# Optimization experiments

Measured on AMD Instinct MI355X. Metric: run time of the kernel, lower is better.

The kernel has to match this reference:

```python
import jax, jax.numpy as jnp
import numpy as np

# Model config (matches init_kwargs)
DIM = 2048
INTER = 1408          # moe_inter_dim
E = 16                # n_routed_experts
TOPK = 4              # n_activated_experts
G = 4                 # n_expert_groups
TOPK_G = 2            # n_limited_groups
N_SHARED = 2
SHARED_INTER = N_SHARED * INTER  # 2816
ROUTE_SCALE = 1.0


def setup_inputs() -> dict:
    key = jax.random.key(0)
    ks = jax.random.split(key, 8)
    s = 0.02
    x = jax.random.normal(ks[0], (1, 2048, DIM), dtype=jnp.float32)
    Wg = jax.random.normal(ks[1], (E, DIM), dtype=jnp.float32) * s      # gate weight
    W1 = jax.random.normal(ks[2], (E, INTER, DIM), dtype=jnp.float32) * s  # expert gate proj
    W3 = jax.random.normal(ks[3], (E, INTER, DIM), dtype=jnp.float32) * s  # expert up proj
    W2 = jax.random.normal(ks[4], (E, DIM, INTER), dtype=jnp.float32) * s  # expert down proj
    Ws1 = jax.random.normal(ks[5], (SHARED_INTER, DIM), dtype=jnp.float32) * s
    Ws3 = jax.random.normal(ks[6], (SHARED_INTER, DIM), dtype=jnp.float32) * s
    Ws2 = jax.random.normal(ks[7], (DIM, SHARED_INTER), dtype=jnp.float32) * s
    return {"x": x, "Wg": Wg, "W1": W1, "W3": W3, "W2": W2,
            "Ws1": Ws1, "Ws3": Ws3, "Ws2": Ws2}


def _moe_forward(x, Wg, W1, W3, W2, Ws1, Ws3, Ws2):
    B, S, D = x.shape
    xt = x.reshape(-1, D)              # [T, D]
    T = xt.shape[0]

    # ---- Gate: group-limited top-k routing (bias is None since dim != 7168) ----
    scores = jax.nn.softmax(xt @ Wg.T, axis=-1)          # [T, E]
    sg = scores.reshape(T, G, E // G)                    # [T, G, E/G]
    group_scores = sg.max(axis=-1)                       # amax per group
    gidx = jax.lax.top_k(group_scores, TOPK_G)[1]        # [T, TOPK_G]
    gmask = jax.nn.one_hot(gidx, G, dtype=jnp.float32).sum(axis=1) > 0  # [T, G] kept groups
    masked = jnp.where(gmask[:, :, None], sg, -jnp.inf).reshape(T, E)
    topi = jax.lax.top_k(masked, TOPK)[1]                # [T, TOPK] expert indices
    weights = jnp.take_along_axis(scores, topi, axis=1) * ROUTE_SCALE  # original_scores gather

    # ---- Routed experts: dense per-expert SwiGLU FFN, zero-weight combine ----
    # combine[t, e] = sum over k of weights[t, k] * (topi[t, k] == e)
    combine = jnp.zeros((T, E), xt.dtype).at[jnp.arange(T)[:, None], topi].add(weights)
    h = jax.nn.silu(jnp.einsum('td,eid->eti', xt, W1)) * jnp.einsum('td,eid->eti', xt, W3)
    expert_out = jnp.einsum('eti,edi->etd', h, W2)       # [E, T, D]
    y = jnp.einsum('etd,te->td', expert_out, combine)    # [T, D]

    # ---- Shared expert (applied to all tokens) ----
    z = (jax.nn.silu(xt @ Ws1.T) * (xt @ Ws3.T)) @ Ws2.T

    return (y + z).reshape(B, S, D)


def reference(x, Wg, W1, W3, W2, Ws1, Ws3, Ws2):
    return _moe_forward(x, Wg, W1, W3, W2, Ws1, Ws3, Ws2)
```

## Files before the change

### kernel.cpp

```cpp
#include <hip/hip_runtime.h>
#include <stdint.h>

#define D_MODEL  2048
#define N_INTER  1408
#define SH_INTER 2816
#define T_TOK    2048
#define NSLOT    (T_TOK * 4)
#define MIB(x)   ((size_t)(x) << 20)

typedef __attribute__((ext_vector_type(8))) short bf16x8;
typedef __attribute__((ext_vector_type(4))) float f32x4;

__device__ __forceinline__ unsigned short f2bf(float f){
  unsigned int b = __builtin_bit_cast(unsigned int, f);
  b = (b + 0x7FFFu + ((b >> 16) & 1u)) >> 16;
  return (unsigned short)b;
}
__device__ __forceinline__ float bf2f(unsigned short h){
  unsigned int b = ((unsigned int)h) << 16;
  return __builtin_bit_cast(float, b);
}

#define GLOAD16(gp, lp) __builtin_amdgcn_global_load_lds( \
    (const __attribute__((address_space(1))) unsigned int*)(gp), \
    (__attribute__((address_space(3))) unsigned int*)(lp), 16, 0, 0)

__global__ void cvt_bf16_kernel(const float* __restrict__ x,
                                unsigned short* __restrict__ o, int n4){
  const int stride = gridDim.x * blockDim.x;
  for (int i = blockIdx.x * blockDim.x + threadIdx.x; i < n4; i += stride){
    const float4 v = ((const float4*)x)[i];
    ushort4 u; u.x = f2bf(v.x); u.y = f2bf(v.y); u.z = f2bf(v.z); u.w = f2bf(v.w);
    ((ushort4*)o)[i] = u;
  }
}

__global__ void gate_kernel(const float* __restrict__ x, const float* __restrict__ Wg,
                            int* __restrict__ cnt, int* __restrict__ list,
                            float* __restrict__ wslot){
  const int t = blockIdx.x;
  const int l = threadIdx.x;
  const int e = l & 15, q = l >> 4;
  const float* xr = x + (size_t)t * D_MODEL + q * 512;
  const float* wr = Wg + (size_t)e * D_MODEL + q * 512;
  float p = 0.f;
  #pragma unroll 4
  for (int i = 0; i < 512; i += 4){
    float4 xv = *(const float4*)(xr + i);
    float4 wv = *(const float4*)(wr + i);
    p += xv.x*wv.x + xv.y*wv.y + xv.z*wv.z + xv.w*wv.w;
  }
  p += __shfl_xor(p, 16);
  p += __shfl_xor(p, 32);
  float mx = p;
  for (int d = 1; d < 16; d <<= 1) mx = fmaxf(mx, __shfl_xor(mx, d));
  float ex = __expf(p - mx);
  float sum = ex;
  for (int d = 1; d < 16; d <<= 1) sum += __shfl_xor(sum, d);
  const float sc = ex / sum;
  float gm = fmaxf(sc, __shfl_xor(sc, 1));
  gm = fmaxf(gm, __shfl_xor(gm, 2));
  const float g0 = __shfl(gm, 0), g1 = __shfl(gm, 4),
              g2 = __shfl(gm, 8), g3 = __shfl(gm, 12);
  const int grp = e >> 2;
  const float gs[4] = {g0, g1, g2, g3};
  int grank = 0;
  #pragma unroll
  for (int j = 0; j < 4; ++j)
    if (gs[j] > gm || (gs[j] == gm && j < grp)) grank++;
  const float msc = (grank < 2) ? sc : -INFINITY;
  int erank = 0;
  #pragma unroll
  for (int j = 0; j < 16; ++j){
    const float oj = __shfl(msc, j);
    if (oj > msc || (oj == msc && j < e)) erank++;
  }
  if (q == 0 && erank < 4 && msc > -INFINITY){
    const int pos = atomicAdd(&cnt[e], 1);
    const int slot = (t << 2) | erank;
    list[e * T_TOK + pos] = slot;
    wslot[slot] = sc;
  }
}

template<int GATHER>
__global__ __launch_bounds__(256, 2)
void gemm_gu_kernel(const unsigned short* __restrict__ A,
                    const unsigned short* __restrict__ BG,
                    const unsigned short* __restrict__ BU,
                    unsigned short* __restrict__ H,
                    const int* __restrict__ list,
                    const int* __restrict__ cnt,
                    int ebase, int K, int NI, int MT, int NT)
{
  __shared__ __align__(128) char smem[24576 + 49152];
  unsigned short* As = (unsigned short*)smem;
  unsigned short* Bs = (unsigned short*)(smem + 24576);
  float* scr = (float*)smem;

  const int per = gridDim.x >> 3;
  const int gsw = (blockIdx.x & 7) * per + (blockIdx.x >> 3);
  const int mt   = gsw % MT;
  const int rest = gsw / MT;
  const int nt = GATHER ? (rest % NT) : rest;
  const int e  = GATHER ? (ebase + rest / NT) : 0;
  const int cntE = GATHER ? cnt[e] : (MT * 128);
  if (mt * 128 >= cntE) return;

  const int tid = threadIdx.x, wid = tid >> 6, lane = tid & 63;
  const int sx = ((lane & 3) ^ ((lane >> 3) & 3)) << 3;

  const int rt0 = 32 * wid + (lane >> 2), rt1 = rt0 + 16;
  int ar0, ar1;
  if (GATHER){
    const int lim = cntE - 1;
    int p0 = mt * 128 + rt0; p0 = p0 < lim ? p0 : lim;
    int p1 = mt * 128 + rt1; p1 = p1 < lim ? p1 : lim;
    ar0 = list[e * T_TOK + p0] >> 2;
    ar1 = list[e * T_TOK + p1] >> 2;
  } else { ar0 = mt * 128 + rt0; ar1 = mt * 128 + rt1; }
  const unsigned short* pa0 = A + (size_t)ar0 * K + sx;
  const unsigned short* pa1 = A + (size_t)ar1 * K + sx;

  const unsigned short* wsrc = (wid < 2) ? BG : BU;
  if (GATHER) wsrc += (size_t)(e - ebase) * NI * K;
  const int rb = (64 * wid + (lane >> 2)) & 127;
  const unsigned short* pb0 = wsrc + (size_t)(nt * 128 + rb     ) * K + sx;
  const unsigned short* pb1 = wsrc + (size_t)(nt * 128 + rb + 16) * K + sx;
  const unsigned short* pb2 = wsrc + (size_t)(nt * 128 + rb + 32) * K + sx;
  const unsigned short* pb3 = wsrc + (size_t)(nt * 128 + rb + 48) * K + sx;

  const int aW0 = (32 * wid) * 32, aW1 = aW0 + 512;
  const int bW  = (64 * wid) * 32;
  const int aStr = 128 * 32, bStr = 256 * 32;

  const int wr = wid >> 1, wc = wid & 1, lr = lane & 15, lq = lane >> 4;
  const int fx = ((lq ^ ((lr >> 1) & 3)) << 3);
  int aoff[4], boff[8];
  #pragma unroll
  for (int m = 0; m < 4; ++m) aoff[m] = (wr * 64 + m * 16 + lr) * 32 + fx;
  #pragma unroll
  for (int n = 0; n < 8; ++n) boff[n] = (wc * 128 + n * 16 + lr) * 32 + fx;

  f32x4 acc[4][8];
  const f32x4 zero = {0.f, 0.f, 0.f, 0.f};
  #pragma unroll
  for (int m = 0; m < 4; ++m)
    #pragma unroll
    for (int n = 0; n < 8; ++n) acc[m][n] = zero;

  const int KT = K >> 5;
  #pragma unroll
  for (int t = 0; t < 3; ++t){
    GLOAD16(pa0, As + t * aStr + aW0);
    GLOAD16(pa1, As + t * aStr + aW1);
    GLOAD16(pb0, Bs + t * bStr + bW);
    GLOAD16(pb1, Bs + t * bStr + bW + 512);
    GLOAD16(pb2, Bs + t * bStr + bW + 1024);
    GLOAD16(pb3, Bs + t * bStr + bW + 1536);
    pa0 += 32; pa1 += 32; pb0 += 32; pb1 += 32; pb2 += 32; pb3 += 32;
  }
  int c = 0;

  for (int kt = 0; kt < KT; ++kt){
    if (kt < KT - 2)       asm volatile("s_waitcnt vmcnt(12)" ::: "memory");
    else if (kt == KT - 2) asm volatile("s_waitcnt vmcnt(6)"  ::: "memory");
    else                   asm volatile("s_waitcnt vmcnt(0)"  ::: "memory");
    __builtin_amdgcn_s_barrier();

    const unsigned short* aC = As + c * aStr;
    const unsigned short* bC = Bs + c * bStr;
    bf16x8 af[4], bf[8];
    #pragma unroll
    for (int m = 0; m < 4; ++m) af[m] = *(const bf16x8*)(aC + aoff[m]);
    #pragma unroll
    for (int n = 0; n < 8; ++n) bf[n] = *(const bf16x8*)(bC + boff[n]);

    asm volatile("s_waitcnt lgkmcnt(0)" ::: "memory");
    __builtin_amdgcn_sched_barrier(0);
    __builtin_amdgcn_s_barrier();

    if (kt + 3 < KT){
      GLOAD16(pa0, As + c * aStr + aW0);
      GLOAD16(pa1, As + c * aStr + aW1);
      GLOAD16(pb0, Bs + c * bStr + bW);
      GLOAD16(pb1, Bs + c * bStr + bW + 512);
      GLOAD16(pb2, Bs + c * bStr + bW + 1024);
      GLOAD16(pb3, Bs + c * bStr + bW + 1536);
      pa0 += 32; pa1 += 32; pb0 += 32; pb1 += 32; pb2 += 32; pb3 += 32;
    }

    #pragma unroll
    for (int n = 0; n < 8; ++n)
      #pragma unroll
      for (int m = 0; m < 4; ++m)
        acc[m][n] = __builtin_amdgcn_mfma_f32_16x16x32_bf16(af[m], bf[n], acc[m][n], 0, 0, 0);

    c = (c == 2) ? 0 : c + 1;
  }

  if (wc == 1){
    #pragma unroll
    for (int m = 0; m < 4; ++m)
      #pragma unroll
      for (int r = 0; r < 4; ++r){
        const int row = m * 16 + lq * 4 + r;
        #pragma unroll
        for (int n = 0; n < 8; ++n){
          const int ucol = (n * 16 + lr) ^ ((lq & 1) << 4);
          scr[wr * 8192 + row * 128 + ucol] = acc[m][n][r];
        }
      }
  }
  __syncthreads();
  if (wc == 0){
    #pragma unroll
    for (int m = 0; m < 4; ++m)
      #pragma unroll
      for (int r = 0; r < 4; ++r){
        const int row = m * 16 + lq * 4 + r;
        const int grow = mt * 128 + wr * 64 + row;
        if (GATHER && grow >= cntE) continue;
        const int orow = GATHER ? list[e * T_TOK + grow] : grow;
        unsigned short* op = H + (size_t)orow * NI + nt * 128;
        #pragma unroll
        for (int n = 0; n < 8; ++n){
          const float g = acc[m][n][r];
          const int ucol = (n * 16 + lr) ^ ((lq & 1) << 4);
          const float u = scr[wr * 8192 + row * 128 + ucol];
          op[n * 16 + lr] = f2bf(g / (1.f + __expf(-g)) * u);
        }
      }
  }
}

template<int GATHER>
__global__ __launch_bounds__(256, 2)
void gemm_down_kernel(const unsigned short* __restrict__ A,
                      const unsigned short* __restrict__ B,
                      void* __restrict__ OutP,
                      const int* __restrict__ list,
                      const int* __restrict__ cnt,
                      int K, int N, int MT, int NT)
{
  __shared__ __align__(128) char smem[24576 + 49152];
  unsigned short* As = (unsigned short*)smem;
  unsigned short* Bs = (unsigned short*)(smem + 24576);

  const int per = gridDim.x >> 3;
  const int gsw = (blockIdx.x & 7) * per + (blockIdx.x >> 3);
  const int mt   = gsw % MT;
  const int rest = gsw / MT;
  const int nt = GATHER ? (rest % NT) : rest;
  const int e  = GATHER ? (rest / NT) : 0;
  const int cntE = GATHER ? cnt[e] : (MT * 128);
  if (mt * 128 >= cntE) return;

  const int tid = threadIdx.x, wid = tid >> 6, lane = tid & 63;
  const int sx = ((lane & 3) ^ ((lane >> 3) & 3)) << 3;

  const int rt0 = 32 * wid + (lane >> 2), rt1 = rt0 + 16;
  int ar0, ar1;
  if (GATHER){
    const int lim = cntE - 1;
    int p0 = mt * 128 + rt0; p0 = p0 < lim ? p0 : lim;
    int p1 = mt * 128 + rt1; p1 = p1 < lim ? p1 : lim;
    ar0 = list[e * T_TOK + p0];
    ar1 = list[e * T_TOK + p1];
  } else { ar0 = mt * 128 + rt0; ar1 = mt * 128 + rt1; }
  const unsigned short* pa0 = A + (size_t)ar0 * K + sx;
  const unsigned short* pa1 = A + (size_t)ar1 * K + sx;

  const unsigned short* wsrc = B + (GATHER ? (size_t)e * N * K : 0);
  const int rb = 64 * wid + (lane >> 2);
  const unsigned short* pb0 = wsrc + (size_t)(nt * 256 + rb     ) * K + sx;
  const unsigned short* pb1 = wsrc + (size_t)(nt * 256 + rb + 16) * K + sx;
  const unsigned short* pb2 = wsrc + (size_t)(nt * 256 + rb + 32) * K + sx;
  const unsigned short* pb3 = wsrc + (size_t)(nt * 256 + rb + 48) * K + sx;

  const int aW0 = (32 * wid) * 32, aW1 = aW0 + 512;
  const int bW  = (64 * wid) * 32;
  const int aStr = 128 * 32, bStr = 256 * 32;

  const int wr = wid >> 1, wc = wid & 1, lr = lane & 15, lq = lane >> 4;
  const int fx = ((lq ^ ((lr >> 1) & 3)) << 3);
  int aoff[4], boff[8];
  #pragma unroll
  for (int m = 0; m < 4; ++m) aoff[m] = (wr * 64 + m * 16 + lr) * 32 + fx;
  #pragma unroll
  for (int n = 0; n < 8; ++n) boff[n] = (wc * 128 + n * 16 + lr) * 32 + fx;

  f32x4 acc[4][8];
  const f32x4 zero = {0.f, 0.f, 0.f, 0.f};
  #pragma unroll
  for (int m = 0; m < 4; ++m)
    #pragma unroll
    for (int n = 0; n < 8; ++n) acc[m][n] = zero;

  const int KT = K >> 5;
  #pragma unroll
  for (int t = 0; t < 3; ++t){
    GLOAD16(pa0, As + t * aStr + aW0);
    GLOAD16(pa1, As + t * aStr + aW1);
    GLOAD16(pb0, Bs + t * bStr + bW);
    GLOAD16(pb1, Bs + t * bStr + bW + 512);
    GLOAD16(pb2, Bs + t * bStr + bW + 1024);
    GLOAD16(pb3, Bs + t * bStr + bW + 1536);
    pa0 += 32; pa1 += 32; pb0 += 32; pb1 += 32; pb2 += 32; pb3 += 32;
  }
  int c = 0;

  for (int kt = 0; kt < KT; ++kt){
    if (kt < KT - 2)       asm volatile("s_waitcnt vmcnt(12)" ::: "memory");
    else if (kt == KT - 2) asm volatile("s_waitcnt vmcnt(6)"  ::: "memory");
    else                   asm volatile("s_waitcnt vmcnt(0)"  ::: "memory");
    __builtin_amdgcn_s_barrier();

    const unsigned short* aC = As + c * aStr;
    const unsigned short* bC = Bs + c * bStr;
    bf16x8 af[4], bf[8];
    #pragma unroll
    for (int m = 0; m < 4; ++m) af[m] = *(const bf16x8*)(aC + aoff[m]);
    #pragma unroll
    for (int n = 0; n < 8; ++n) bf[n] = *(const bf16x8*)(bC + boff[n]);

    asm volatile("s_waitcnt lgkmcnt(0)" ::: "memory");
    __builtin_amdgcn_sched_barrier(0);
    __builtin_amdgcn_s_barrier();

    if (kt + 3 < KT){
      GLOAD16(pa0, As + c * aStr + aW0);
      GLOAD16(pa1, As + c * aStr + aW1);
      GLOAD16(pb0, Bs + c * bStr + bW);
      GLOAD16(pb1, Bs + c * bStr + bW + 512);
      GLOAD16(pb2, Bs + c * bStr + bW + 1024);
      GLOAD16(pb3, Bs + c * bStr + bW + 1536);
      pa0 += 32; pa1 += 32; pb0 += 32; pb1 += 32; pb2 += 32; pb3 += 32;
    }

    #pragma unroll
    for (int n = 0; n < 8; ++n)
      #pragma unroll
      for (int m = 0; m < 4; ++m)
        acc[m][n] = __builtin_amdgcn_mfma_f32_16x16x32_bf16(af[m], bf[n], acc[m][n], 0, 0, 0);

    c = (c == 2) ? 0 : c + 1;
  }

  const int colBase = nt * 256 + wc * 128;
  #pragma unroll
  for (int m = 0; m < 4; ++m){
    #pragma unroll
    for (int r = 0; r < 4; ++r){
      const int grow = mt * 128 + wr * 64 + m * 16 + lq * 4 + r;
      if (GATHER == 0){
        float* op = (float*)OutP + (size_t)grow * N + colBase;
        #pragma unroll
        for (int n = 0; n < 8; ++n) op[n * 16 + lr] = acc[m][n][r];
      } else {
        if (grow >= cntE) continue;
        const int orow = list[e * T_TOK + grow];
        unsigned short* op = (unsigned short*)OutP + (size_t)orow * N + colBase;
        #pragma unroll
        for (int n = 0; n < 8; ++n) op[n * 16 + lr] = f2bf(acc[m][n][r]);
      }
    }
  }
}

__global__ void combine_kernel(const unsigned short* __restrict__ H2,
                               const float* __restrict__ wslot,
                               float* __restrict__ out){
  const int t = blockIdx.x;
  const int ccol = threadIdx.x * 8;
  float w[4];
  #pragma unroll
  for (int k = 0; k < 4; ++k) w[k] = wslot[t * 4 + k];
  float* o = out + (size_t)t * D_MODEL + ccol;
  float a[8];
  #pragma unroll
  for (int j = 0; j < 8; ++j) a[j] = o[j];
  #pragma unroll
  for (int k = 0; k < 4; ++k){
    const bf16x8 hv = *(const bf16x8*)(H2 + (size_t)(t * 4 + k) * D_MODEL + ccol);
    #pragma unroll
    for (int j = 0; j < 8; ++j) a[j] += w[k] * bf2f((unsigned short)hv[j]);
  }
  #pragma unroll
  for (int j = 0; j < 8; ++j) o[j] = a[j];
}

extern "C" void kernel_launch(void* const* d_in, const int* in_sizes, int n_in,
                              void* d_out, int out_size, void* d_ws, size_t ws_size,
                              hipStream_t stream)
{
  const float* x   = (const float*)d_in[0];
  const float* Wg  = (const float*)d_in[1];
  const float* W1  = (const float*)d_in[2];
  const float* W3  = (const float*)d_in[3];
  const float* W2  = (const float*)d_in[4];
  const float* Ws1 = (const float*)d_in[5];
  const float* Ws3 = (const float*)d_in[6];
  const float* Ws2 = (const float*)d_in[7];
  float* out = (float*)d_out;

  char* ws = (char*)d_ws;
  int*   cnt   = (int*)(ws);
  int*   list  = (int*)(ws + 4096);
  float* wslot = (float*)(ws + 4096 + 131072);
  unsigned short* xbf = (unsigned short*)(ws + MIB(1));
  unsigned short* H2  = (unsigned short*)(ws + MIB(1));
  unsigned short* Hs  = (unsigned short*)(ws + MIB(10));
  unsigned short* Hr  = (unsigned short*)(ws + MIB(34));
  unsigned short* WA  = (unsigned short*)(ws + MIB(57));
  unsigned short* WB  = (unsigned short*)(ws + MIB(101));

  hipMemsetAsync(cnt, 0, 4096, stream);
  cvt_bf16_kernel<<<2048, 256, 0, stream>>>(x, xbf, T_TOK * D_MODEL / 4);
  gate_kernel<<<T_TOK, 64, 0, stream>>>(x, Wg, cnt, list, wslot);

  cvt_bf16_kernel<<<2048, 256, 0, stream>>>(Ws1, WA, SH_INTER * D_MODEL / 4);
  cvt_bf16_kernel<<<2048, 256, 0, stream>>>(Ws3, WB, SH_INTER * D_MODEL / 4);
  gemm_gu_kernel<0><<<16 * 22, 256, 0, stream>>>(xbf, WA, WB, Hs, nullptr, nullptr,
                                                 0, D_MODEL, SH_INTER, 16, 22);
  cvt_bf16_kernel<<<2048, 256, 0, stream>>>(Ws2, WA, D_MODEL * SH_INTER / 4);
  gemm_down_kernel<0><<<16 * 8, 256, 0, stream>>>(Hs, WA, out, nullptr, nullptr,
                                                  SH_INTER, D_MODEL, 16, 8);

  for (int h = 0; h < 2; ++h){
    const size_t wOff = (size_t)(8 * h) * N_INTER * D_MODEL;
    cvt_bf16_kernel<<<4096, 256, 0, stream>>>(W1 + wOff, WA, (int)(8u * N_INTER * D_MODEL / 4));
    cvt_bf16_kernel<<<4096, 256, 0, stream>>>(W3 + wOff, WB, (int)(8u * N_INTER * D_MODEL / 4));
    gemm_gu_kernel<1><<<16 * 11 * 8, 256, 0, stream>>>(xbf, WA, WB, Hr, list, cnt,
                                                       8 * h, D_MODEL, N_INTER, 16, 11);
  }
  cvt_bf16_kernel<<<8192, 256, 0, stream>>>(W2, WA, 16 * D_MODEL * N_INTER / 4);
  gemm_down_kernel<1><<<16 * 8 * 16, 256, 0, stream>>>(Hr, WA, H2, list, cnt,
                                                       N_INTER, D_MODEL, 16, 8);
  combine_kernel<<<T_TOK, 256, 0, stream>>>(H2, wslot, out);
}
```

Measured before the change: 640.4 us.

## Split-K shared down GEMM, fuse expert launches, separate gate/up tiles

The shared-expert down GEMM is split into four K slices writing fp32 partials that the combine kernel sums, raising block count to fill the GPU. Routed-expert weight conversion and the gate/up GEMM now run for all 16 experts in one launch instead of two halves. The gate/up kernel computes gate and up for the same 64 columns per wave, so SiLU*up can be applied without an LDS exchange and extra barrier. MFMA loops get raised wave priority. The cost is a larger workspace and extra partial-sum traffic in the combine kernel.

```diff
diff --git a/kernel.cpp b/kernel.cpp
--- a/kernel.cpp
+++ b/kernel.cpp
@@ -85,25 +85,24 @@
 
 template<int GATHER>
 __global__ __launch_bounds__(256, 2)
-void gemm_gu_kernel(const unsigned short* __restrict__ A,
-                    const unsigned short* __restrict__ BG,
-                    const unsigned short* __restrict__ BU,
-                    unsigned short* __restrict__ H,
-                    const int* __restrict__ list,
-                    const int* __restrict__ cnt,
-                    int ebase, int K, int NI, int MT, int NT)
+void gemm_gu2_kernel(const unsigned short* __restrict__ A,
+                     const unsigned short* __restrict__ BG,
+                     const unsigned short* __restrict__ BU,
+                     unsigned short* __restrict__ H,
+                     const int* __restrict__ list,
+                     const int* __restrict__ cnt,
+                     int K, int NI, int MT, int NT)
 {
-  __shared__ __align__(128) char smem[24576 + 49152];
-  unsigned short* As = (unsigned short*)smem;
-  unsigned short* Bs = (unsigned short*)(smem + 24576);
-  float* scr = (float*)smem;
+  __shared__ unsigned short As [3 * 4096];
+  __shared__ unsigned short BsG[3 * 4096];
+  __shared__ unsigned short BsU[3 * 4096];
 
   const int per = gridDim.x >> 3;
   const int gsw = (blockIdx.x & 7) * per + (blockIdx.x >> 3);
   const int mt   = gsw % MT;
   const int rest = gsw / MT;
   const int nt = GATHER ? (rest % NT) : rest;
-  const int e  = GATHER ? (ebase + rest / NT) : 0;
+  const int e  = GATHER ? (rest / NT) : 0;
   const int cntE = GATHER ? cnt[e] : (MT * 128);
   if (mt * 128 >= cntE) return;
 
@@ -122,43 +121,40 @@
   const unsigned short* pa0 = A + (size_t)ar0 * K + sx;
   const unsigned short* pa1 = A + (size_t)ar1 * K + sx;
 
-  const unsigned short* wsrc = (wid < 2) ? BG : BU;
-  if (GATHER) wsrc += (size_t)(e - ebase) * NI * K;
-  const int rb = (64 * wid + (lane >> 2)) & 127;
-  const unsigned short* pb0 = wsrc + (size_t)(nt * 128 + rb     ) * K + sx;
-  const unsigned short* pb1 = wsrc + (size_t)(nt * 128 + rb + 16) * K + sx;
-  const unsigned short* pb2 = wsrc + (size_t)(nt * 128 + rb + 32) * K + sx;
-  const unsigned short* pb3 = wsrc + (size_t)(nt * 128 + rb + 48) * K + sx;
-
-  const int aW0 = (32 * wid) * 32, aW1 = aW0 + 512;
-  const int bW  = (64 * wid) * 32;
-  const int aStr = 128 * 32, bStr = 256 * 32;
+  const size_t eoff = GATHER ? (size_t)e * NI * K : 0;
+  const unsigned short* pg0 = BG + eoff + (size_t)(nt * 128 + rt0) * K + sx;
+  const unsigned short* pg1 = pg0 + (size_t)16 * K;
+  const unsigned short* pu0 = BU + eoff + (size_t)(nt * 128 + rt0) * K + sx;
+  const unsigned short* pu1 = pu0 + (size_t)16 * K;
+
+  const int w0 = (32 * wid) * 32, w1 = w0 + 512;
+  const int bufStr = 4096;
 
   const int wr = wid >> 1, wc = wid & 1, lr = lane & 15, lq = lane >> 4;
   const int fx = ((lq ^ ((lr >> 1) & 3)) << 3);
-  int aoff[4], boff[8];
+  int aoff[4], boff[4];
   #pragma unroll
   for (int m = 0; m < 4; ++m) aoff[m] = (wr * 64 + m * 16 + lr) * 32 + fx;
   #pragma unroll
-  for (int n = 0; n < 8; ++n) boff[n] = (wc * 128 + n * 16 + lr) * 32 + fx;
-
-  f32x4 acc[4][8];
+  for (int n = 0; n < 4; ++n) boff[n] = (wc * 64 + n * 16 + lr) * 32 + fx;
+
+  f32x4 accg[4][4], accu[4][4];
   const f32x4 zero = {0.f, 0.f, 0.f, 0.f};
   #pragma unroll
   for (int m = 0; m < 4; ++m)
     #pragma unroll
-    for (int n = 0; n < 8; ++n) acc[m][n] = zero;
+    for (int n = 0; n < 4; ++n){ accg[m][n] = zero; accu[m][n] = zero; }
 
   const int KT = K >> 5;
   #pragma unroll
   for (int t = 0; t < 3; ++t){
-    GLOAD16(pa0, As + t * aStr + aW0);
-    GLOAD16(pa1, As + t * aStr + aW1);
-    GLOAD16(pb0, Bs + t * bStr + bW);
-    GLOAD16(pb1, Bs + t * bStr + bW + 512);
-    GLOAD16(pb2, Bs + t * bStr + bW + 1024);
-    GLOAD16(pb3, Bs + t * bStr + bW + 1536);
-    pa0 += 32; pa1 += 32; pb0 += 32; pb1 += 32; pb2 += 32; pb3 += 32;
+    GLOAD16(pa0, As  + t * bufStr + w0);
+    GLOAD16(pa1, As  + t * bufStr + w1);
+    GLOAD16(pg0, BsG + t * bufStr + w0);
+    GLOAD16(pg1, BsG + t * bufStr + w1);
+    GLOAD16(pu0, BsU + t * bufStr + w0);
+    GLOAD16(pu1, BsU + t * bufStr + w1);
+    pa0 += 32; pa1 += 32; pg0 += 32; pg1 += 32; pu0 += 32; pu1 += 32;
   }
   int c = 0;
 
@@ -168,73 +164,63 @@
     else                   asm volatile("s_waitcnt vmcnt(0)"  ::: "memory");
     __builtin_amdgcn_s_barrier();
 
-    const unsigned short* aC = As + c * aStr;
-    const unsigned short* bC = Bs + c * bStr;
-    bf16x8 af[4], bf[8];
+    const unsigned short* aC = As  + c * bufStr;
+    const unsigned short* gC = BsG + c * bufStr;
+    const unsigned short* uC = BsU + c * bufStr;
+    bf16x8 af[4], bg[4], bu[4];
     #pragma unroll
     for (int m = 0; m < 4; ++m) af[m] = *(const bf16x8*)(aC + aoff[m]);
     #pragma unroll
-    for (int n = 0; n < 8; ++n) bf[n] = *(const bf16x8*)(bC + boff[n]);
+    for (int n = 0; n < 4; ++n) bg[n] = *(const bf16x8*)(gC + boff[n]);
+    #pragma unroll
+    for (int n = 0; n < 4; ++n) bu[n] = *(const bf16x8*)(uC + boff[n]);
 
     asm volatile("s_waitcnt lgkmcnt(0)" ::: "memory");
     __builtin_amdgcn_sched_barrier(0);
     __builtin_amdgcn_s_barrier();
 
     if (kt + 3 < KT){
-      GLOAD16(pa0, As + c * aStr + aW0);
-      GLOAD16(pa1, As + c * aStr + aW1);
-      GLOAD16(pb0, Bs + c * bStr + bW);
-      GLOAD16(pb1, Bs + c * bStr + bW + 512);
-      GLOAD16(pb2, Bs + c * bStr + bW + 1024);
-      GLOAD16(pb3, Bs + c * bStr + bW + 1536);
-      pa0 += 32; pa1 += 32; pb0 += 32; pb1 += 32; pb2 += 32; pb3 += 32;
+      GLOAD16(pa0, As  + c * bufStr + w0);
+      GLOAD16(pa1, As  + c * bufStr + w1);
+      GLOAD16(pg0, BsG + c * bufStr + w0);
+      GLOAD16(pg1, BsG + c * bufStr + w1);
+      GLOAD16(pu0, BsU + c * bufStr + w0);
+      GLOAD16(pu1, BsU + c * bufStr + w1);
+      pa0 += 32; pa1 += 32; pg0 += 32; pg1 += 32; pu0 += 32; pu1 += 32;
     }
 
-    #pragma unroll
-    for (int n = 0; n < 8; ++n)
+    __builtin_amdgcn_s_setprio(1);
+    #pragma unroll
+    for (int n = 0; n < 4; ++n)
       #pragma unroll
-      for (int m = 0; m < 4; ++m)
-        acc[m][n] = __builtin_amdgcn_mfma_f32_16x16x32_bf16(af[m], bf[n], acc[m][n], 0, 0, 0);
+      for (int m = 0; m < 4; ++m){
+        accg[m][n] = __builtin_amdgcn_mfma_f32_16x16x32_bf16(af[m], bg[n], accg[m][n], 0, 0, 0);
+        accu[m][n] = __builtin_amdgcn_mfma_f32_16x16x32_bf16(af[m], bu[n], accu[m][n], 0, 0, 0);
+      }
+    __builtin_amdgcn_s_setprio(0);
 
     c = (c == 2) ? 0 : c + 1;
   }
 
-  if (wc == 1){
-    #pragma unroll
-    for (int m = 0; m < 4; ++m)
+  const int colBase = nt * 128 + wc * 64;
+  #pragma unroll
+  for (int m = 0; m < 4; ++m){
+    #pragma unroll
+    for (int r = 0; r < 4; ++r){
+      const int grow = mt * 128 + wr * 64 + m * 16 + lq * 4 + r;
+      if (GATHER && grow >= cntE) continue;
+      const int orow = GATHER ? list[e * T_TOK + grow] : grow;
+      unsigned short* op = H + (size_t)orow * NI + colBase;
       #pragma unroll
-      for (int r = 0; r < 4; ++r){
-        const int row = m * 16 + lq * 4 + r;
-        #pragma unroll
-        for (int n = 0; n < 8; ++n){
-          const int ucol = (n * 16 + lr) ^ ((lq & 1) << 4);
-          scr[wr * 8192 + row * 128 + ucol] = acc[m][n][r];
-        }
+      for (int n = 0; n < 4; ++n){
+        const float g = accg[m][n][r], u = accu[m][n][r];
+        op[n * 16 + lr] = f2bf(g / (1.f + __expf(-g)) * u);
       }
-  }
-  __syncthreads();
-  if (wc == 0){
-    #pragma unroll
-    for (int m = 0; m < 4; ++m)
-      #pragma unroll
-      for (int r = 0; r < 4; ++r){
-        const int row = m * 16 + lq * 4 + r;
-        const int grow = mt * 128 + wr * 64 + row;
-        if (GATHER && grow >= cntE) continue;
-        const int orow = GATHER ? list[e * T_TOK + grow] : grow;
-        unsigned short* op = H + (size_t)orow * NI + nt * 128;
-        #pragma unroll
-        for (int n = 0; n < 8; ++n){
-          const float g = acc[m][n][r];
-          const int ucol = (n * 16 + lr) ^ ((lq & 1) << 4);
-          const float u = scr[wr * 8192 + row * 128 + ucol];
-          op[n * 16 + lr] = f2bf(g / (1.f + __expf(-g)) * u);
-        }
-      }
-  }
-}
-
-template<int GATHER>
+    }
+  }
+}
+
+template<int GATHER, int KS>
 __global__ __launch_bounds__(256, 2)
 void gemm_down_kernel(const unsigned short* __restrict__ A,
                       const unsigned short* __restrict__ B,
@@ -250,14 +236,16 @@
   const int per = gridDim.x >> 3;
   const int gsw = (blockIdx.x & 7) * per + (blockIdx.x >> 3);
   const int mt   = gsw % MT;
-  const int rest = gsw / MT;
-  const int nt = GATHER ? (rest % NT) : rest;
-  const int e  = GATHER ? (rest / NT) : 0;
+  int rest = gsw / MT;
+  const int nt = rest % NT; rest /= NT;
+  const int ks = (KS > 1) ? (rest % KS) : 0;
+  const int e  = GATHER ? (rest / (KS > 1 ? KS : 1)) : 0;
   const int cntE = GATHER ? cnt[e] : (MT * 128);
   if (mt * 128 >= cntE) return;
 
   const int tid = threadIdx.x, wid = tid >> 6, lane = tid & 63;
   const int sx = ((lane & 3) ^ ((lane >> 3) & 3)) << 3;
+  const int kOff = ks * (K / KS);
 
   const int rt0 = 32 * wid + (lane >> 2), rt1 = rt0 + 16;
   int ar0, ar1;
@@ -268,10 +256,10 @@
     ar0 = list[e * T_TOK + p0];
     ar1 = list[e * T_TOK + p1];
   } else { ar0 = mt * 128 + rt0; ar1 = mt * 128 + rt1; }
-  const unsigned short* pa0 = A + (size_t)ar0 * K + sx;
-  const unsigned short* pa1 = A + (size_t)ar1 * K + sx;
-
-  const unsigned short* wsrc = B + (GATHER ? (size_t)e * N * K : 0);
+  const unsigned short* pa0 = A + (size_t)ar0 * K + kOff + sx;
+  const unsigned short* pa1 = A + (size_t)ar1 * K + kOff + sx;
+
+  const unsigned short* wsrc = B + (GATHER ? (size_t)e * N * K : 0) + kOff;
   const int rb = 64 * wid + (lane >> 2);
   const unsigned short* pb0 = wsrc + (size_t)(nt * 256 + rb     ) * K + sx;
   const unsigned short* pb1 = wsrc + (size_t)(nt * 256 + rb + 16) * K + sx;
@@ -297,7 +285,7 @@
     #pragma unroll
     for (int n = 0; n < 8; ++n) acc[m][n] = zero;
 
-  const int KT = K >> 5;
+  const int KT = (K / KS) >> 5;
   #pragma unroll
   for (int t = 0; t < 3; ++t){
     GLOAD16(pa0, As + t * aStr + aW0);
@@ -338,11 +326,13 @@
       pa0 += 32; pa1 += 32; pb0 += 32; pb1 += 32; pb2 += 32; pb3 += 32;
     }
 
+    __builtin_amdgcn_s_setprio(1);
     #pragma unroll
     for (int n = 0; n < 8; ++n)
       #pragma unroll
       for (int m = 0; m < 4; ++m)
         acc[m][n] = __builtin_amdgcn_mfma_f32_16x16x32_bf16(af[m], bf[n], acc[m][n], 0, 0, 0);
+    __builtin_amdgcn_s_setprio(0);
 
     c = (c == 2) ? 0 : c + 1;
   }
@@ -354,7 +344,7 @@
     for (int r = 0; r < 4; ++r){
       const int grow = mt * 128 + wr * 64 + m * 16 + lq * 4 + r;
       if (GATHER == 0){
-        float* op = (float*)OutP + (size_t)grow * N + colBase;
+        float* op = (float*)OutP + (size_t)ks * MT * 128 * N + (size_t)grow * N + colBase;
         #pragma unroll
         for (int n = 0; n < 8; ++n) op[n * 16 + lr] = acc[m][n][r];
       } else {
@@ -369,6 +359,7 @@
 }
 
 __global__ void combine_kernel(const unsigned short* __restrict__ H2,
+                               const float* __restrict__ P,
                                const float* __restrict__ wslot,
                                float* __restrict__ out){
   const int t = blockIdx.x;
@@ -376,16 +367,22 @@
   float w[4];
   #pragma unroll
   for (int k = 0; k < 4; ++k) w[k] = wslot[t * 4 + k];
-  float* o = out + (size_t)t * D_MODEL + ccol;
   float a[8];
   #pragma unroll
-  for (int j = 0; j < 8; ++j) a[j] = o[j];
+  for (int j = 0; j < 8; ++j) a[j] = 0.f;
+  #pragma unroll
+  for (int p = 0; p < 4; ++p){
+    const float* pp = P + (size_t)(p * T_TOK + t) * D_MODEL + ccol;
+    #pragma unroll
+    for (int j = 0; j < 8; ++j) a[j] += pp[j];
+  }
   #pragma unroll
   for (int k = 0; k < 4; ++k){
     const bf16x8 hv = *(const bf16x8*)(H2 + (size_t)(t * 4 + k) * D_MODEL + ccol);
     #pragma unroll
     for (int j = 0; j < 8; ++j) a[j] += w[k] * bf2f((unsigned short)hv[j]);
   }
+  float* o = out + (size_t)t * D_MODEL + ccol;
   #pragma unroll
   for (int j = 0; j < 8; ++j) o[j] = a[j];
 }
@@ -410,10 +407,11 @@
   float* wslot = (float*)(ws + 4096 + 131072);
   unsigned short* xbf = (unsigned short*)(ws + MIB(1));
   unsigned short* H2  = (unsigned short*)(ws + MIB(1));
-  unsigned short* Hs  = (unsigned short*)(ws + MIB(10));
-  unsigned short* Hr  = (unsigned short*)(ws + MIB(34));
-  unsigned short* WA  = (unsigned short*)(ws + MIB(57));
-  unsigned short* WB  = (unsigned short*)(ws + MIB(101));
+  unsigned short* Hs  = (unsigned short*)(ws + MIB(34));
+  unsigned short* Hr  = (unsigned short*)(ws + MIB(46));
+  float*          P   = (float*)        (ws + MIB(70));
+  unsigned short* WA  = (unsigned short*)(ws + MIB(138));
+  unsigned short* WB  = (unsigned short*)(ws + MIB(231));
 
   hipMemsetAsync(cnt, 0, 4096, stream);
   cvt_bf16_kernel<<<2048, 256, 0, stream>>>(x, xbf, T_TOK * D_MODEL / 4);
@@ -421,21 +419,18 @@
 
   cvt_bf16_kernel<<<2048, 256, 0, stream>>>(Ws1, WA, SH_INTER * D_MODEL / 4);
   cvt_bf16_kernel<<<2048, 256, 0, stream>>>(Ws3, WB, SH_INTER * D_MODEL / 4);
-  gemm_gu_kernel<0><<<16 * 22, 256, 0, stream>>>(xbf, WA, WB, Hs, nullptr, nullptr,
-                                                 0, D_MODEL, SH_INTER, 16, 22);
+  gemm_gu2_kernel<0><<<16 * 22, 256, 0, stream>>>(xbf, WA, WB, Hs, nullptr, nullptr,
+                                                  D_MODEL, SH_INTER, 16, 22);
   cvt_bf16_kernel<<<2048, 256, 0, stream>>>(Ws2, WA, D_MODEL * SH_INTER / 4);
-  gemm_down_kernel<0><<<16 * 8, 256, 0, stream>>>(Hs, WA, out, nullptr, nullptr,
-                                                  SH_INTER, D_MODEL, 16, 8);
-
-  for (int h = 0; h < 2; ++h){
-    const size_t wOff = (size_t)(8 * h) * N_INTER * D_MODEL;
-    cvt_bf16_kernel<<<4096, 256, 0, stream>>>(W1 + wOff, WA, (int)(8u * N_INTER * D_MODEL / 4));
-    cvt_bf16_kernel<<<4096, 256, 0, stream>>>(W3 + wOff, WB, (int)(8u * N_INTER * D_MODEL / 4));
-    gemm_gu_kernel<1><<<16 * 11 * 8, 256, 0, stream>>>(xbf, WA, WB, Hr, list, cnt,
-                                                       8 * h, D_MODEL, N_INTER, 16, 11);
-  }
+  gemm_down_kernel<0, 4><<<16 * 8 * 4, 256, 0, stream>>>(Hs, WA, P, nullptr, nullptr,
+                                                         SH_INTER, D_MODEL, 16, 8);
+
+  cvt_bf16_kernel<<<8192, 256, 0, stream>>>(W1, WA, 16 * N_INTER * D_MODEL / 4);
+  cvt_bf16_kernel<<<8192, 256, 0, stream>>>(W3, WB, 16 * N_INTER * D_MODEL / 4);
+  gemm_gu2_kernel<1><<<16 * 11 * 16, 256, 0, stream>>>(xbf, WA, WB, Hr, list, cnt,
+                                                       D_MODEL, N_INTER, 16, 11);
   cvt_bf16_kernel<<<8192, 256, 0, stream>>>(W2, WA, 16 * D_MODEL * N_INTER / 4);
-  gemm_down_kernel<1><<<16 * 8 * 16, 256, 0, stream>>>(Hr, WA, H2, list, cnt,
-                                                       N_INTER, D_MODEL, 16, 8);
-  combine_kernel<<<T_TOK, 256, 0, stream>>>(H2, wslot, out);
-}
+  gemm_down_kernel<1, 1><<<16 * 8 * 16, 256, 0, stream>>>(Hr, WA, H2, list, cnt,
+                                                          N_INTER, D_MODEL, 16, 8);
+  combine_kernel<<<T_TOK, 256, 0, stream>>>(H2, P, wslot, out);
+}
```

After: 613.1 us. 4.3% less time.
